# Performance work log

Measured on AMD Instinct MI355X. Metric: run time of the kernel, lower is better.

## Reference

```python
import jax, jax.numpy as jnp
import numpy as np

B, D = 16384, 2048          # batch, input_dim
N_TOP, N_CLASS = 8, 16      # top labels, bottom labels per top (uniform, contiguous ids)

def setup_inputs() -> dict:
    key = jax.random.key(0)
    k1, k2, k3, k4, k5 = jax.random.split(key, 5)
    INIT = 0.2  # matches init_weight uniform(-0.2, 0.2)
    return {
        "features": jax.random.normal(k1, (B, D), dtype=jnp.float32),
        "top_W": jax.random.uniform(k2, (N_TOP, D), minval=-INIT, maxval=INIT, dtype=jnp.float32),
        "top_b": jax.random.uniform(k3, (N_TOP,), minval=-INIT, maxval=INIT, dtype=jnp.float32),
        "bottom_W": jax.random.uniform(k4, (N_TOP, D, N_CLASS), minval=-INIT, maxval=INIT, dtype=jnp.float32),
        "bottom_b": jax.random.uniform(k5, (N_TOP, N_CLASS), minval=-INIT, maxval=INIT, dtype=jnp.float32),
    }

def reference(features, top_W, top_b, bottom_W, bottom_b):
    # dropout p=0.0 -> identity
    # top gate: linear + sigmoid, (b, n_top)
    top_scores = jax.nn.sigmoid(features @ top_W.T + top_b)
    # all per-top-label expert linears as one batched GEMM: (b, n_top, n_class)
    bottom_logits = jnp.einsum('bd,tdc->btc', features, bottom_W) + bottom_b
    bottom_scores = jax.nn.softmax(bottom_logits, axis=-1)
    # scatter-combine: bottom ids of top i are contiguous [i*N_CLASS, (i+1)*N_CLASS),
    # so the column scatter is a reshape. (b, n_bottom_labels)
    final_scores = (top_scores[:, :, None] * bottom_scores).reshape(features.shape[0], N_TOP * N_CLASS)
    return final_scores
```

## Files before the change

### kernel.cpp

```cpp
#include <hip/hip_runtime.h>


#define D_DIM 2048
#define NTILE 9
#define M_ROWS 32

using f32x4 = float __attribute__((ext_vector_type(4)));
using half8 = _Float16 __attribute__((ext_vector_type(8)));
using fp16x2 = __fp16 __attribute__((ext_vector_type(2)));

__global__ void prep_weights(const float* __restrict__ topW,
                             const float* __restrict__ botW,
                             _Float16* __restrict__ S) {
    int idx = blockIdx.x * blockDim.x + threadIdx.x;
    if (idx >= 4 * 16 * NTILE * 64) return;
    int lane = idx & 63;
    int tmp  = idx >> 6;
    int nt   = tmp % NTILE;
    int wks  = tmp / NTILE;
    int n     = nt * 16 + (lane & 15);
    int kbase = wks * 32 + (lane >> 4) * 8;

    _Float16 v[8];
    #pragma unroll
    for (int j = 0; j < 8; j++) {
        int k = kbase + j;
        float x = 0.0f;
        if (n < 8) {
            x = topW[n * D_DIM + k];
        } else if (n < 136) {
            int t = (n - 8) >> 4, c = (n - 8) & 15;
            x = botW[(t * D_DIM + k) * 16 + c];
        }
        v[j] = (_Float16)x;
    }
    *(half8*)(S + (size_t)idx * 8) = *(half8*)v;
}

static __device__ __forceinline__ half8 pack_af(f32x4 a, f32x4 b) {
    fp16x2 p0 = __builtin_amdgcn_cvt_pkrtz(a[0], a[1]);
    fp16x2 p1 = __builtin_amdgcn_cvt_pkrtz(a[2], a[3]);
    fp16x2 p2 = __builtin_amdgcn_cvt_pkrtz(b[0], b[1]);
    fp16x2 p3 = __builtin_amdgcn_cvt_pkrtz(b[2], b[3]);
    half8 r;
    r[0] = (_Float16)p0[0]; r[1] = (_Float16)p0[1];
    r[2] = (_Float16)p1[0]; r[3] = (_Float16)p1[1];
    r[4] = (_Float16)p2[0]; r[5] = (_Float16)p2[1];
    r[6] = (_Float16)p3[0]; r[7] = (_Float16)p3[1];
    return r;
}

__global__ __launch_bounds__(256, 2) void hc_fused(
        const float* __restrict__ feat, const _Float16* __restrict__ Bsw,
        const float* __restrict__ top_b, const float* __restrict__ bot_b,
        float* __restrict__ out) {
    __shared__ float red[4][M_ROWS][148];

    const int tid  = threadIdx.x;
    const int lane = tid & 63, wave = tid >> 6;
    const int quad = lane >> 4, low = lane & 15;
    const size_t row0 = (size_t)blockIdx.x * M_ROWS;

    const float* A0 = feat + (row0 + low) * D_DIM + wave * 512 + quad * 8;
    const float* A1 = A0 + 16 * D_DIM;
    const _Float16* Bp = Bsw + (size_t)wave * (16 * NTILE * 512) + lane * 8;

    f32x4 acc0[NTILE], acc1[NTILE];
    #pragma unroll
    for (int i = 0; i < NTILE; i++) { acc0[i] = (f32x4)0.0f; acc1[i] = (f32x4)0.0f; }

    half8 bB0[NTILE], bB1[NTILE];
    f32x4 bA0[4], bA1[4], bA2[4], bA3[4];

#define LOAD_B(SET, KS) do {                                               \
        const _Float16* Bn_ = Bp + (size_t)(KS) * NTILE * 512;             \
        _Pragma("unroll")                                                  \
        for (int nt_ = 0; nt_ < NTILE; nt_++)                              \
            SET[nt_] = *(const half8*)(Bn_ + nt_ * 512);                   \
    } while (0)

#define LOAD_A(SET, KS) do {                                               \
        const float* a0_ = A0 + (KS) * 32;                                 \
        const float* a1_ = A1 + (KS) * 32;                                 \
        SET[0] = *(const f32x4*)(a0_);                                     \
        SET[1] = *(const f32x4*)(a0_ + 4);                                 \
        SET[2] = *(const f32x4*)(a1_);                                     \
        SET[3] = *(const f32x4*)(a1_ + 4);                                 \
    } while (0)

#define COMPUTE(ASET, BSET) do {                                           \
        const half8 af0_ = pack_af(ASET[0], ASET[1]);                      \
        const half8 af1_ = pack_af(ASET[2], ASET[3]);                      \
        _Pragma("unroll")                                                  \
        for (int nt_ = 0; nt_ < NTILE; nt_++) {                            \
            acc0[nt_] = __builtin_amdgcn_mfma_f32_16x16x32_f16(            \
                            af0_, BSET[nt_], acc0[nt_], 0, 0, 0);          \
            acc1[nt_] = __builtin_amdgcn_mfma_f32_16x16x32_f16(            \
                            af1_, BSET[nt_], acc1[nt_], 0, 0, 0);          \
        }                                                                  \
    } while (0)

    LOAD_B(bB0, 0);  LOAD_A(bA0, 0);
    LOAD_B(bB1, 1);  LOAD_A(bA1, 1);  LOAD_A(bA2, 2);

    COMPUTE(bA0, bB0);  LOAD_B(bB0,  2);  LOAD_A(bA3,  3);
    COMPUTE(bA1, bB1);  LOAD_B(bB1,  3);  LOAD_A(bA0,  4);
    COMPUTE(bA2, bB0);  LOAD_B(bB0,  4);  LOAD_A(bA1,  5);
    COMPUTE(bA3, bB1);  LOAD_B(bB1,  5);  LOAD_A(bA2,  6);
    COMPUTE(bA0, bB0);  LOAD_B(bB0,  6);  LOAD_A(bA3,  7);
    COMPUTE(bA1, bB1);  LOAD_B(bB1,  7);  LOAD_A(bA0,  8);
    COMPUTE(bA2, bB0);  LOAD_B(bB0,  8);  LOAD_A(bA1,  9);
    COMPUTE(bA3, bB1);  LOAD_B(bB1,  9);  LOAD_A(bA2, 10);
    COMPUTE(bA0, bB0);  LOAD_B(bB0, 10);  LOAD_A(bA3, 11);
    COMPUTE(bA1, bB1);  LOAD_B(bB1, 11);  LOAD_A(bA0, 12);
    COMPUTE(bA2, bB0);  LOAD_B(bB0, 12);  LOAD_A(bA1, 13);
    COMPUTE(bA3, bB1);  LOAD_B(bB1, 13);  LOAD_A(bA2, 14);
    COMPUTE(bA0, bB0);  LOAD_B(bB0, 14);  LOAD_A(bA3, 15);
    COMPUTE(bA1, bB1);  LOAD_B(bB1, 15);
    COMPUTE(bA2, bB0);
    COMPUTE(bA3, bB1);

#undef LOAD_B
#undef LOAD_A
#undef COMPUTE

    #pragma unroll
    for (int nt = 0; nt < NTILE; nt++) {
        #pragma unroll
        for (int r = 0; r < 4; r++) {
            red[wave][quad * 4 + r][nt * 16 + low]      = acc0[nt][r];
            red[wave][16 + quad * 4 + r][nt * 16 + low] = acc1[nt][r];
        }
    }
    __syncthreads();

    const int row = tid >> 3;
    const int top = tid & 7;
    {
        float zt = top_b[top];
        #pragma unroll
        for (int w = 0; w < 4; w++) zt += red[w][row][top];
        const float sig = 1.0f / (1.0f + __expf(-zt));

        float z[16];
        float zmax = -1e30f;
        #pragma unroll
        for (int c = 0; c < 16; c++) {
            float v = bot_b[top * 16 + c];
            #pragma unroll
            for (int w = 0; w < 4; w++) v += red[w][row][8 + top * 16 + c];
            z[c] = v;
            zmax = fmaxf(zmax, v);
        }
        float s = 0.0f;
        #pragma unroll
        for (int c = 0; c < 16; c++) { z[c] = __expf(z[c] - zmax); s += z[c]; }
        const float scale = sig / s;

        float* o = out + (row0 + row) * 128 + top * 16;
        #pragma unroll
        for (int c = 0; c < 16; c += 4) {
            f32x4 v = { z[c] * scale, z[c+1] * scale, z[c+2] * scale, z[c+3] * scale };
            *(f32x4*)(o + c) = v;
        }
    }
}

extern "C" void kernel_launch(void* const* d_in, const int* in_sizes, int n_in,
                              void* d_out, int out_size, void* d_ws, size_t ws_size,
                              hipStream_t stream) {
    const float* feat  = (const float*)d_in[0];
    const float* topW  = (const float*)d_in[1];
    const float* topB  = (const float*)d_in[2];
    const float* botW  = (const float*)d_in[3];
    const float* botB  = (const float*)d_in[4];
    float* out = (float*)d_out;
    _Float16* Bsw = (_Float16*)d_ws;

    prep_weights<<<(4 * 16 * NTILE * 64 + 255) / 256, 256, 0, stream>>>(topW, botW, Bsw);
    hc_fused<<<16384 / M_ROWS, 256, 0, stream>>>(feat, Bsw, topB, botB, out);
}
```

Before: 212.5 us.

## Halve rows per block to 16 and simplify pipeline for higher occupancy

Each block now handles 16 rows instead of 32, so every wave keeps a single set of accumulators and loads B fragments per step instead of double-buffering them. Only A is prefetched one step ahead, and launch bounds rise from 2 to 4 blocks per SM to use the lower register count. The cost is that each B fragment is reused across half as many rows, so total weight reads from L2 double, and prefetch depth is shallower. Only 128 threads do the epilogue.

```diff
diff --git a/kernel.cpp b/kernel.cpp
--- a/kernel.cpp
+++ b/kernel.cpp
@@ -3,7 +3,7 @@
 
 #define D_DIM 2048
 #define NTILE 9
-#define M_ROWS 32
+#define M_ROWS 16
 
 using f32x4 = float __attribute__((ext_vector_type(4)));
 using half8 = _Float16 __attribute__((ext_vector_type(8)));
@@ -50,7 +50,7 @@
     return r;
 }
 
-__global__ __launch_bounds__(256, 2) void hc_fused(
+__global__ __launch_bounds__(256, 4) void hc_fused(
         const float* __restrict__ feat, const _Float16* __restrict__ Bsw,
         const float* __restrict__ top_b, const float* __restrict__ bot_b,
         float* __restrict__ out) {
@@ -62,81 +62,74 @@
     const size_t row0 = (size_t)blockIdx.x * M_ROWS;
 
     const float* A0 = feat + (row0 + low) * D_DIM + wave * 512 + quad * 8;
-    const float* A1 = A0 + 16 * D_DIM;
     const _Float16* Bp = Bsw + (size_t)wave * (16 * NTILE * 512) + lane * 8;
 
-    f32x4 acc0[NTILE], acc1[NTILE];
+    f32x4 acc[NTILE];
     #pragma unroll
-    for (int i = 0; i < NTILE; i++) { acc0[i] = (f32x4)0.0f; acc1[i] = (f32x4)0.0f; }
+    for (int i = 0; i < NTILE; i++) acc[i] = (f32x4)0.0f;
 
-    half8 bB0[NTILE], bB1[NTILE];
-    f32x4 bA0[4], bA1[4], bA2[4], bA3[4];
+    f32x4 aC0, aC1, aN0, aN1;
+    aC0 = *(const f32x4*)(A0);
+    aC1 = *(const f32x4*)(A0 + 4);
 
-#define LOAD_B(SET, KS) do {                                               \
+#define STEP(KS, AL0, AL1, NL0, NL1) do {                                  \
         const _Float16* Bn_ = Bp + (size_t)(KS) * NTILE * 512;             \
-        _Pragma("unroll")                                                  \
-        for (int nt_ = 0; nt_ < NTILE; nt_++)                              \
-            SET[nt_] = *(const half8*)(Bn_ + nt_ * 512);                   \
+        half8 b0_ = *(const half8*)(Bn_);                                  \
+        half8 b1_ = *(const half8*)(Bn_ + 1 * 512);                        \
+        half8 b2_ = *(const half8*)(Bn_ + 2 * 512);                        \
+        half8 b3_ = *(const half8*)(Bn_ + 3 * 512);                        \
+        half8 b4_ = *(const half8*)(Bn_ + 4 * 512);                        \
+        half8 b5_ = *(const half8*)(Bn_ + 5 * 512);                        \
+        half8 b6_ = *(const half8*)(Bn_ + 6 * 512);                        \
+        half8 b7_ = *(const half8*)(Bn_ + 7 * 512);                        \
+        half8 b8_ = *(const half8*)(Bn_ + 8 * 512);                        \
+        if ((KS) < 15) {                                                   \
+            NL0 = *(const f32x4*)(A0 + ((KS) + 1) * 32);                   \
+            NL1 = *(const f32x4*)(A0 + ((KS) + 1) * 32 + 4);               \
+        }                                                                  \
+        const half8 af_ = pack_af(AL0, AL1);                               \
+        acc[0] = __builtin_amdgcn_mfma_f32_16x16x32_f16(af_, b0_, acc[0], 0, 0, 0); \
+        acc[1] = __builtin_amdgcn_mfma_f32_16x16x32_f16(af_, b1_, acc[1], 0, 0, 0); \
+        acc[2] = __builtin_amdgcn_mfma_f32_16x16x32_f16(af_, b2_, acc[2], 0, 0, 0); \
+        acc[3] = __builtin_amdgcn_mfma_f32_16x16x32_f16(af_, b3_, acc[3], 0, 0, 0); \
+        acc[4] = __builtin_amdgcn_mfma_f32_16x16x32_f16(af_, b4_, acc[4], 0, 0, 0); \
+        acc[5] = __builtin_amdgcn_mfma_f32_16x16x32_f16(af_, b5_, acc[5], 0, 0, 0); \
+        acc[6] = __builtin_amdgcn_mfma_f32_16x16x32_f16(af_, b6_, acc[6], 0, 0, 0); \
+        acc[7] = __builtin_amdgcn_mfma_f32_16x16x32_f16(af_, b7_, acc[7], 0, 0, 0); \
+        acc[8] = __builtin_amdgcn_mfma_f32_16x16x32_f16(af_, b8_, acc[8], 0, 0, 0); \
     } while (0)
 
-#define LOAD_A(SET, KS) do {                                               \
-        const float* a0_ = A0 + (KS) * 32;                                 \
-        const float* a1_ = A1 + (KS) * 32;                                 \
-        SET[0] = *(const f32x4*)(a0_);                                     \
-        SET[1] = *(const f32x4*)(a0_ + 4);                                 \
-        SET[2] = *(const f32x4*)(a1_);                                     \
-        SET[3] = *(const f32x4*)(a1_ + 4);                                 \
-    } while (0)
-
-#define COMPUTE(ASET, BSET) do {                                           \
-        const half8 af0_ = pack_af(ASET[0], ASET[1]);                      \
-        const half8 af1_ = pack_af(ASET[2], ASET[3]);                      \
-        _Pragma("unroll")                                                  \
-        for (int nt_ = 0; nt_ < NTILE; nt_++) {                            \
-            acc0[nt_] = __builtin_amdgcn_mfma_f32_16x16x32_f16(            \
-                            af0_, BSET[nt_], acc0[nt_], 0, 0, 0);          \
-            acc1[nt_] = __builtin_amdgcn_mfma_f32_16x16x32_f16(            \
-                            af1_, BSET[nt_], acc1[nt_], 0, 0, 0);          \
-        }                                                                  \
-    } while (0)
-
-    LOAD_B(bB0, 0);  LOAD_A(bA0, 0);
-    LOAD_B(bB1, 1);  LOAD_A(bA1, 1);  LOAD_A(bA2, 2);
-
-    COMPUTE(bA0, bB0);  LOAD_B(bB0,  2);  LOAD_A(bA3,  3);
-    COMPUTE(bA1, bB1);  LOAD_B(bB1,  3);  LOAD_A(bA0,  4);
-    COMPUTE(bA2, bB0);  LOAD_B(bB0,  4);  LOAD_A(bA1,  5);
-    COMPUTE(bA3, bB1);  LOAD_B(bB1,  5);  LOAD_A(bA2,  6);
-    COMPUTE(bA0, bB0);  LOAD_B(bB0,  6);  LOAD_A(bA3,  7);
-    COMPUTE(bA1, bB1);  LOAD_B(bB1,  7);  LOAD_A(bA0,  8);
-    COMPUTE(bA2, bB0);  LOAD_B(bB0,  8);  LOAD_A(bA1,  9);
-    COMPUTE(bA3, bB1);  LOAD_B(bB1,  9);  LOAD_A(bA2, 10);
-    COMPUTE(bA0, bB0);  LOAD_B(bB0, 10);  LOAD_A(bA3, 11);
-    COMPUTE(bA1, bB1);  LOAD_B(bB1, 11);  LOAD_A(bA0, 12);
-    COMPUTE(bA2, bB0);  LOAD_B(bB0, 12);  LOAD_A(bA1, 13);
-    COMPUTE(bA3, bB1);  LOAD_B(bB1, 13);  LOAD_A(bA2, 14);
-    COMPUTE(bA0, bB0);  LOAD_B(bB0, 14);  LOAD_A(bA3, 15);
-    COMPUTE(bA1, bB1);  LOAD_B(bB1, 15);
-    COMPUTE(bA2, bB0);
-    COMPUTE(bA3, bB1);
-
-#undef LOAD_B
-#undef LOAD_A
-#undef COMPUTE
+    STEP( 0, aC0, aC1, aN0, aN1);
+    STEP( 1, aN0, aN1, aC0, aC1);
+    STEP( 2, aC0, aC1, aN0, aN1);
+    STEP( 3, aN0, aN1, aC0, aC1);
+    STEP( 4, aC0, aC1, aN0, aN1);
+    STEP( 5, aN0, aN1, aC0, aC1);
+    STEP( 6, aC0, aC1, aN0, aN1);
+    STEP( 7, aN0, aN1, aC0, aC1);
+    STEP( 8, aC0, aC1, aN0, aN1);
+    STEP( 9, aN0, aN1, aC0, aC1);
+    STEP(10, aC0, aC1, aN0, aN1);
+    STEP(11, aN0, aN1, aC0, aC1);
+    STEP(12, aC0, aC1, aN0, aN1);
+    STEP(13, aN0, aN1, aC0, aC1);
+    STEP(14, aC0, aC1, aN0, aN1);
+    STEP(15, aN0, aN1, aC0, aC1);
+#undef STEP
 
     #pragma unroll
     for (int nt = 0; nt < NTILE; nt++) {
         #pragma unroll
         for (int r = 0; r < 4; r++) {
-            red[wave][quad * 4 + r][nt * 16 + low]      = acc0[nt][r];
-            red[wave][16 + quad * 4 + r][nt * 16 + low] = acc1[nt][r];
+            red[wave][quad * 4 + r][nt * 16 + low] = acc[nt][r];
         }
     }
     __syncthreads();
 
-    const int row = tid >> 3;
-    const int top = tid & 7;
-    {
+    if (tid < 128) {
+        const int row = tid >> 3;
+        const int top = tid & 7;
+
         float zt = top_b[top];
         #pragma unroll
         for (int w = 0; w < 4; w++) zt += red[w][row][top];
```

Measured after the change: 226.5 us. +6.6%, slower.

## Split K across blocks with LDS-staged weights and separate epilogue kernel

Applied to the files above, without the earlier changes.

The fused kernel is restructured so each block handles 128 rows by a quarter of K, with each wave taking 32 rows. Weight chunks are double-buffered into LDS via global_load_lds and shared by all four waves, instead of every wave streaming its own weights from global memory. Partial sums go to a global workspace, and a new epilogue kernel reduces the four K-quarters and applies sigmoid and softmax. This cuts redundant weight traffic and register pressure, but adds a partial-sum round trip (about 38 MB written and read) and an extra kernel launch.

```diff
diff --git a/kernel.cpp b/kernel.cpp
--- a/kernel.cpp
+++ b/kernel.cpp
@@ -3,7 +3,8 @@
 
 #define D_DIM 2048
 #define NTILE 9
-#define M_ROWS 32
+#define CH_B 36864
+#define NCHUNK 16
 
 using f32x4 = float __attribute__((ext_vector_type(4)));
 using half8 = _Float16 __attribute__((ext_vector_type(8)));
@@ -13,13 +14,15 @@
                              const float* __restrict__ botW,
                              _Float16* __restrict__ S) {
     int idx = blockIdx.x * blockDim.x + threadIdx.x;
-    if (idx >= 4 * 16 * NTILE * 64) return;
+    if (idx >= NCHUNK * 4 * NTILE * 64) return;
     int lane = idx & 63;
-    int tmp  = idx >> 6;
-    int nt   = tmp % NTILE;
-    int wks  = tmp / NTILE;
+    int t1   = idx >> 6;
+    int nt   = t1 % NTILE;
+    int t2   = t1 / NTILE;
+    int kf   = t2 & 3;
+    int chunk= t2 >> 2;
     int n     = nt * 16 + (lane & 15);
-    int kbase = wks * 32 + (lane >> 4) * 8;
+    int kbase = chunk * 128 + kf * 32 + (lane >> 4) * 8;
 
     _Float16 v[8];
     #pragma unroll
@@ -50,119 +53,130 @@
     return r;
 }
 
-__global__ __launch_bounds__(256, 2) void hc_fused(
-        const float* __restrict__ feat, const _Float16* __restrict__ Bsw,
-        const float* __restrict__ top_b, const float* __restrict__ bot_b,
-        float* __restrict__ out) {
-    __shared__ float red[4][M_ROWS][148];
+typedef __attribute__((address_space(1))) const void gv_t;
+typedef __attribute__((address_space(3))) void lv_t;
+
+__global__ __launch_bounds__(256, 2) void hc_main(
+        const float* __restrict__ feat, const _Float16* __restrict__ S,
+        float* __restrict__ P) {
+    __shared__ _Float16 buf[2][CH_B / 2];
 
     const int tid  = threadIdx.x;
     const int lane = tid & 63, wave = tid >> 6;
     const int quad = lane >> 4, low = lane & 15;
-    const size_t row0 = (size_t)blockIdx.x * M_ROWS;
+    const int rg = blockIdx.x & 127, kq = blockIdx.x >> 7;
+    const int row0 = rg * 128 + wave * 32;
 
-    const float* A0 = feat + (row0 + low) * D_DIM + wave * 512 + quad * 8;
-    const float* A1 = A0 + 16 * D_DIM;
-    const _Float16* Bp = Bsw + (size_t)wave * (16 * NTILE * 512) + lane * 8;
+    const char* gB = (const char*)S + (size_t)(kq * 4) * CH_B;
+    const char* lB = (const char*)&buf[0][0];
+
+    const float* Ar = feat + (size_t)(row0 + low) * D_DIM + kq * 512 + quad * 8;
 
     f32x4 acc0[NTILE], acc1[NTILE];
     #pragma unroll
     for (int i = 0; i < NTILE; i++) { acc0[i] = (f32x4)0.0f; acc1[i] = (f32x4)0.0f; }
 
-    half8 bB0[NTILE], bB1[NTILE];
-    f32x4 bA0[4], bA1[4], bA2[4], bA3[4];
-
-#define LOAD_B(SET, KS) do {                                               \
-        const _Float16* Bn_ = Bp + (size_t)(KS) * NTILE * 512;             \
+#define STAGE(SLOT, CH) do {                                               \
+        const char* g_ = gB + (CH) * CH_B + (unsigned)(tid * 16);          \
         _Pragma("unroll")                                                  \
-        for (int nt_ = 0; nt_ < NTILE; nt_++)                              \
-            SET[nt_] = *(const half8*)(Bn_ + nt_ * 512);                   \
-    } while (0)
-
-#define LOAD_A(SET, KS) do {                                               \
-        const float* a0_ = A0 + (KS) * 32;                                 \
-        const float* a1_ = A1 + (KS) * 32;                                 \
-        SET[0] = *(const f32x4*)(a0_);                                     \
-        SET[1] = *(const f32x4*)(a0_ + 4);                                 \
-        SET[2] = *(const f32x4*)(a1_);                                     \
-        SET[3] = *(const f32x4*)(a1_ + 4);                                 \
-    } while (0)
-
-#define COMPUTE(ASET, BSET) do {                                           \
-        const half8 af0_ = pack_af(ASET[0], ASET[1]);                      \
-        const half8 af1_ = pack_af(ASET[2], ASET[3]);                      \
-        _Pragma("unroll")                                                  \
-        for (int nt_ = 0; nt_ < NTILE; nt_++) {                            \
-            acc0[nt_] = __builtin_amdgcn_mfma_f32_16x16x32_f16(            \
-                            af0_, BSET[nt_], acc0[nt_], 0, 0, 0);          \
-            acc1[nt_] = __builtin_amdgcn_mfma_f32_16x16x32_f16(            \
-                            af1_, BSET[nt_], acc1[nt_], 0, 0, 0);          \
+        for (int r_ = 0; r_ < 9; r_++) {                                   \
+            __builtin_amdgcn_global_load_lds(                              \
+                (gv_t*)(g_ + r_ * 4096),                                   \
+                (lv_t*)(lB + (SLOT) * CH_B + wave * 1024 + r_ * 4096),     \
+                16, 0, 0);                                                 \
         }                                                                  \
     } while (0)
 
-    LOAD_B(bB0, 0);  LOAD_A(bA0, 0);
-    LOAD_B(bB1, 1);  LOAD_A(bA1, 1);  LOAD_A(bA2, 2);
+#define STEPBODY(S_) do {                                                  \
+        const float* a_ = Ar + (S_) * 128;                                 \
+        f32x4 aA[4], aB[4], aC[4], aD[4];                                  \
+        _Pragma("unroll")                                                  \
+        for (int kf = 0; kf < 4; kf++) {                                   \
+            aA[kf] = *(const f32x4*)(a_ + kf * 32);                        \
+            aB[kf] = *(const f32x4*)(a_ + kf * 32 + 4);                    \
+            aC[kf] = *(const f32x4*)(a_ + 16 * D_DIM + kf * 32);           \
+            aD[kf] = *(const f32x4*)(a_ + 16 * D_DIM + kf * 32 + 4);       \
+        }                                                                  \
+        _Pragma("unroll")                                                  \
+        for (int kf = 0; kf < 4; kf++) {                                   \
+            const half8 af0 = pack_af(aA[kf], aB[kf]);                     \
+            const half8 af1 = pack_af(aC[kf], aD[kf]);                     \
+            const _Float16* Lp = (const _Float16*)(lB + ((S_) & 1) * CH_B) \
+                                 + kf * 4608 + lane * 8;                   \
+            _Pragma("unroll")                                              \
+            for (int nt = 0; nt < NTILE; nt++) {                           \
+                half8 bf = *(const half8*)(Lp + nt * 512);                 \
+                acc0[nt] = __builtin_amdgcn_mfma_f32_16x16x32_f16(         \
+                               af0, bf, acc0[nt], 0, 0, 0);                \
+                acc1[nt] = __builtin_amdgcn_mfma_f32_16x16x32_f16(         \
+                               af1, bf, acc1[nt], 0, 0, 0);                \
+            }                                                              \
+        }                                                                  \
+    } while (0)
 
-    COMPUTE(bA0, bB0);  LOAD_B(bB0,  2);  LOAD_A(bA3,  3);
-    COMPUTE(bA1, bB1);  LOAD_B(bB1,  3);  LOAD_A(bA0,  4);
-    COMPUTE(bA2, bB0);  LOAD_B(bB0,  4);  LOAD_A(bA1,  5);
-    COMPUTE(bA3, bB1);  LOAD_B(bB1,  5);  LOAD_A(bA2,  6);
-    COMPUTE(bA0, bB0);  LOAD_B(bB0,  6);  LOAD_A(bA3,  7);
-    COMPUTE(bA1, bB1);  LOAD_B(bB1,  7);  LOAD_A(bA0,  8);
-    COMPUTE(bA2, bB0);  LOAD_B(bB0,  8);  LOAD_A(bA1,  9);
-    COMPUTE(bA3, bB1);  LOAD_B(bB1,  9);  LOAD_A(bA2, 10);
-    COMPUTE(bA0, bB0);  LOAD_B(bB0, 10);  LOAD_A(bA3, 11);
-    COMPUTE(bA1, bB1);  LOAD_B(bB1, 11);  LOAD_A(bA0, 12);
-    COMPUTE(bA2, bB0);  LOAD_B(bB0, 12);  LOAD_A(bA1, 13);
-    COMPUTE(bA3, bB1);  LOAD_B(bB1, 13);  LOAD_A(bA2, 14);
-    COMPUTE(bA0, bB0);  LOAD_B(bB0, 14);  LOAD_A(bA3, 15);
-    COMPUTE(bA1, bB1);  LOAD_B(bB1, 15);
-    COMPUTE(bA2, bB0);
-    COMPUTE(bA3, bB1);
+    STAGE(0, 0); __syncthreads();
+    STAGE(1, 1); STEPBODY(0); __syncthreads();
+    STAGE(0, 2); STEPBODY(1); __syncthreads();
+    STAGE(1, 3); STEPBODY(2); __syncthreads();
+    STEPBODY(3);
 
-#undef LOAD_B
-#undef LOAD_A
-#undef COMPUTE
+#undef STAGE
+#undef STEPBODY
 
+    float* Pp = P + ((size_t)kq * 16384 + row0) * 144;
     #pragma unroll
     for (int nt = 0; nt < NTILE; nt++) {
         #pragma unroll
         for (int r = 0; r < 4; r++) {
-            red[wave][quad * 4 + r][nt * 16 + low]      = acc0[nt][r];
-            red[wave][16 + quad * 4 + r][nt * 16 + low] = acc1[nt][r];
+            Pp[(quad * 4 + r) * 144 + nt * 16 + low]        = acc0[nt][r];
+            Pp[(16 + quad * 4 + r) * 144 + nt * 16 + low]   = acc1[nt][r];
         }
     }
-    __syncthreads();
+}
 
-    const int row = tid >> 3;
-    const int top = tid & 7;
-    {
-        float zt = top_b[top];
+__global__ __launch_bounds__(256) void hc_epi(
+        const float* __restrict__ P, const float* __restrict__ top_b,
+        const float* __restrict__ bot_b, float* __restrict__ out) {
+    const int gt  = blockIdx.x * 256 + threadIdx.x;
+    const int row = gt >> 3;
+    const int top = gt & 7;
+    const size_t KQS = (size_t)16384 * 144;
+    const float* p0 = P + (size_t)row * 144;
+
+    float zt = top_b[top] + p0[top] + p0[KQS + top]
+             + p0[2 * KQS + top] + p0[3 * KQS + top];
+    const float sig = 1.0f / (1.0f + __expf(-zt));
+
+    const int cb = 8 + top * 16;
+    f32x4 zv[4];
+    #pragma unroll
+    for (int i = 0; i < 4; i++) zv[i] = *(const f32x4*)(bot_b + top * 16 + i * 4);
+    #pragma unroll
+    for (int q = 0; q < 4; q++) {
+        const float* pq = p0 + q * KQS + cb;
         #pragma unroll
-        for (int w = 0; w < 4; w++) zt += red[w][row][top];
-        const float sig = 1.0f / (1.0f + __expf(-zt));
+        for (int i = 0; i < 4; i++) zv[i] += *(const f32x4*)(pq + i * 4);
+    }
 
-        float z[16];
-        float zmax = -1e30f;
+    float zmax = -1e30f;
+    #pragma unroll
+    for (int i = 0; i < 4; i++)
         #pragma unroll
-        for (int c = 0; c < 16; c++) {
-            float v = bot_b[top * 16 + c];
-            #pragma unroll
-            for (int w = 0; w < 4; w++) v += red[w][row][8 + top * 16 + c];
-            z[c] = v;
-            zmax = fmaxf(zmax, v);
-        }
-        float s = 0.0f;
+        for (int j = 0; j < 4; j++) zmax = fmaxf(zmax, zv[i][j]);
+
+    float s = 0.0f;
+    #pragma unroll
+    for (int i = 0; i < 4; i++)
         #pragma unroll
-        for (int c = 0; c < 16; c++) { z[c] = __expf(z[c] - zmax); s += z[c]; }
-        const float scale = sig / s;
+        for (int j = 0; j < 4; j++) { zv[i][j] = __expf(zv[i][j] - zmax); s += zv[i][j]; }
+    const float scale = sig / s;
 
-        float* o = out + (row0 + row) * 128 + top * 16;
-        #pragma unroll
-        for (int c = 0; c < 16; c += 4) {
-            f32x4 v = { z[c] * scale, z[c+1] * scale, z[c+2] * scale, z[c+3] * scale };
-            *(f32x4*)(o + c) = v;
-        }
+    float* o = out + (size_t)row * 128 + top * 16;
+    #pragma unroll
+    for (int i = 0; i < 4; i++) {
+        f32x4 v = { zv[i][0] * scale, zv[i][1] * scale,
+                    zv[i][2] * scale, zv[i][3] * scale };
+        *(f32x4*)(o + i * 4) = v;
     }
 }
 
@@ -175,8 +189,11 @@
     const float* botW  = (const float*)d_in[3];
     const float* botB  = (const float*)d_in[4];
     float* out = (float*)d_out;
+
     _Float16* Bsw = (_Float16*)d_ws;
+    float* P = (float*)((char*)d_ws + (1 << 20));
 
-    prep_weights<<<(4 * 16 * NTILE * 64 + 255) / 256, 256, 0, stream>>>(topW, botW, Bsw);
-    hc_fused<<<16384 / M_ROWS, 256, 0, stream>>>(feat, Bsw, topB, botB, out);
+    prep_weights<<<(NCHUNK * 4 * NTILE * 64 + 255) / 256, 256, 0, stream>>>(topW, botW, Bsw);
+    hc_main<<<512, 256, 0, stream>>>(feat, Bsw, P);
+    hc_epi<<<512, 256, 0, stream>>>(P, topB, botB, out);
 }
```

Result: slower. 222.9 us (+4.9%).
